# Performance work log

Measured on AMD Instinct MI355X. Metric: run time of the kernel, lower is better.

Reference implementation:

```python
import jax, jax.numpy as jnp
import numpy as np

KERNEL_SIZE = 9
DOMAIN = 8
VTH1 = 1.0
VTH2 = 1.0
VTH3 = 100000.0
BETA1 = min(0.999, 0.9)
BETA2 = min(0.999, 0.9)
BETA3 = min(0.999, 0.95)


def _make_kernels() -> np.ndarray:
    # 16 oriented Gaussian kernels, sigma1=1, sigma2=4, phi = k*2*pi/32, k=0..15
    ks = []
    a = np.linspace(-DOMAIN, DOMAIN, KERNEL_SIZE)
    xs, ys = np.meshgrid(a, a, indexing='xy')  # centered at (0,0)
    coo = np.stack([xs, ys], axis=2)  # [K,K,2]
    l1, l2 = 1.0 ** 2, 4.0 ** 2
    for count in range(16):
        phi = count * 2.0 * np.pi / 32.0
        c, s = np.cos(phi), np.sin(phi)
        cxx = l1 * c * c + l2 * s * s
        cxy = (l1 - l2) * c * s
        cyy = l1 * s * s + l2 * c * c
        cov = np.array([[cxx, cxy], [cxy, cyy]])
        ci = np.linalg.inv(cov)
        cd = np.linalg.det(cov)
        frac = 1.0 / (2.0 * np.pi * np.sqrt(cd))
        # quadratic form: (-coo) @ ci . coo  (matches torch einsum chain)
        q = np.einsum('xyj,jk,xyk->xy', -coo, ci, coo)
        ks.append(frac * np.exp(q / 2.0))
    return np.stack(ks).astype(np.float32)[:, None]  # [16,1,9,9]


def heaviside(v):
    return (v > 0).astype(v.dtype)


def setup_inputs() -> dict:
    key = jax.random.key(0)
    k1, k2, k3 = jax.random.split(key, 3)
    B, T, H, W = 16, 50, 64, 64
    x = jax.random.uniform(k1, (B, T, 1, H, W), dtype=jnp.float32)
    kernels = jnp.asarray(_make_kernels())  # [16,1,9,9], fixed buffer
    fan1 = 16 * H * W
    w1 = jax.random.uniform(k2, (200, fan1), jnp.float32, -1.0, 1.0) / np.sqrt(fan1)
    w2 = jax.random.uniform(k3, (1, 200), jnp.float32, -1.0, 1.0) / np.sqrt(200.0)
    return {"x": x, "kernels": kernels, "w1": w1, "w2": w2}


def reference(x, kernels, w1, w2):
    B, T, C, H, W = x.shape
    pad = KERNEL_SIZE // 2

    def step(carry, xt):
        m1, m2, m3 = carry
        # conv2d, stride 1, same padding -> [B,16,H,W]
        g1 = jax.lax.conv_general_dilated(
            xt, kernels, window_strides=(1, 1),
            padding=[(pad, pad), (pad, pad)],
            dimension_numbers=('NCHW', 'OIHW', 'NCHW'))
        # snntorch Leaky, reset_mechanism='zero': reset from previous mem,
        # then mem = (beta*mem + input) * (1 - reset); spk = H(mem - vth)
        r1 = heaviside(m1 - VTH1)
        m1 = (BETA1 * m1 + g1) * (1.0 - r1)
        z1 = heaviside(m1 - VTH1)
        g2 = z1.reshape(B, -1) @ w1.T  # [B,200]
        r2 = heaviside(m2 - VTH2)
        m2 = (BETA2 * m2 + g2) * (1.0 - r2)
        z2 = heaviside(m2 - VTH2)
        g3 = z2 @ w2.T  # [B,1]
        r3 = heaviside(m3 - VTH3)  # threshold 1e5: never fires
        m3 = (BETA3 * m3 + g3) * (1.0 - r3)
        return (m1, m2, m3), m3

    m1 = jnp.zeros((B, 16, H, W), x.dtype)
    m2 = jnp.zeros((B, 200), x.dtype)
    m3 = jnp.zeros((B, 1), x.dtype)
    xt = jnp.moveaxis(x, 1, 0)  # [T,B,1,H,W]
    _, ys = jax.lax.scan(step, (m1, m2, m3), xt)
    return jnp.moveaxis(ys, 0, 1)  # [B,T,1]
```

## Files before the change

### kernel.cpp

```cpp
#include <hip/hip_runtime.h>
#include <hip/hip_bf16.h>


typedef __attribute__((ext_vector_type(8))) short short8;
typedef __attribute__((ext_vector_type(4))) float f32x4;
typedef __attribute__((ext_vector_type(4))) int   i32x4;

#define B_   16
#define T_   50
#define HW_  4096
#define K1N  65536
#define M_   800
#define N2_  200
#define NP_  256
#define KSPL 64
#define BM2  64
#define BK2  64
#define KCH  (K1N / KSPL)
#define MT2  13
#define SW   84
#define NCONV 512
#define NPERM (200 * 32)

static __device__ __forceinline__ short8 mk8(uint a, uint b, uint c, uint d){
  union { uint u[4]; short8 v; } x;
  x.u[0] = a; x.u[1] = b; x.u[2] = c; x.u[3] = d;
  return x.v;
}
static __device__ __forceinline__ uint fnl(uint a, uint b){ return (a >> 16) | (b << 16); }

template<bool WODD>
static __device__ __forceinline__ void rd5(const uint* p, int dw, uint e[5]){
  if (WODD){
    e[0] = p[dw];
    uint2 a = *(const uint2*)(p + dw + 1);
    uint2 b = *(const uint2*)(p + dw + 3);
    e[1] = a.x; e[2] = a.y; e[3] = b.x; e[4] = b.y;
  } else {
    uint2 a = *(const uint2*)(p + dw);
    uint2 b = *(const uint2*)(p + dw + 2);
    e[0] = a.x; e[1] = a.y; e[2] = b.x; e[3] = b.y;
    e[4] = p[dw + 4];
  }
}

template<bool WODD>
static __device__ __forceinline__ void conv_phase(const uint* T0, const uint* T1,
                                                  int bdw,
                                                  const short8 (&afh)[5],
                                                  const short8 (&afl)[5],
                                                  f32x4& acc0, f32x4& acc1){
  #pragma unroll
  for (int ks = 0; ks < 5; ++ks){
    const int dw = bdw + (SW / 2) * 2 * ks;
    uint h[5], m[5];
    rd5<WODD>(T0, dw, h);
    rd5<WODD>(T1, dw, m);
    short8 bh0 = mk8(h[0], h[1], h[2], h[3]);
    short8 bm0 = mk8(m[0], m[1], m[2], m[3]);
    acc0 = __builtin_amdgcn_mfma_f32_16x16x32_bf16(afh[ks], bh0, acc0, 0, 0, 0);
    acc0 = __builtin_amdgcn_mfma_f32_16x16x32_bf16(afh[ks], bm0, acc0, 0, 0, 0);
    acc0 = __builtin_amdgcn_mfma_f32_16x16x32_bf16(afl[ks], bh0, acc0, 0, 0, 0);
    short8 bh1 = mk8(fnl(h[0], h[1]), fnl(h[1], h[2]), fnl(h[2], h[3]), fnl(h[3], h[4]));
    short8 bm1 = mk8(fnl(m[0], m[1]), fnl(m[1], m[2]), fnl(m[2], m[3]), fnl(m[3], m[4]));
    acc1 = __builtin_amdgcn_mfma_f32_16x16x32_bf16(afh[ks], bh1, acc1, 0, 0, 0);
    acc1 = __builtin_amdgcn_mfma_f32_16x16x32_bf16(afh[ks], bm1, acc1, 0, 0, 0);
    acc1 = __builtin_amdgcn_mfma_f32_16x16x32_bf16(afl[ks], bh1, acc1, 0, 0, 0);
  }
}

__global__ __launch_bounds__(256) void k01_fused(const float* __restrict__ x,
                                                 const float* __restrict__ kern,
                                                 const float* __restrict__ w1,
                                                 unsigned char* __restrict__ zout,
                                                 char* __restrict__ wa,
                                                 char* __restrict__ wb){
  __shared__ __align__(16) ushort smem[9152];
  const int bid = blockIdx.x;
  const int tid = threadIdx.x;

  if (bid >= NCONV){
    char* la = (char*)smem;
    char* lb = la + 2048;
    const int bid2 = bid - NCONV;
    const int n = bid2 >> 5;
    const int strip = bid2 & 31;
    #pragma unroll
    for (int i = 0; i < 8; ++i){
      int lin = tid + 256 * i;
      int ch = lin >> 7, p128 = lin & 127;
      float v = w1[(size_t)n * K1N + ch * 4096 + strip * 128 + p128];
      int s = p128 >> 3, o = p128 & 7, q = ch >> 2, r = ch & 3;
      int kp = o * 256 + s * 16 + q * 4 + r;
      float af = rintf(v * 16384.f);
      float rr = v - af * 0x1p-14f;
      float bf = rintf(rr * 0x1p22f);
      int A = (int)af, Bq = (int)bf;
      if (Bq == 128){ A += 1; Bq = -128; }
      la[kp] = (char)A;
      lb[kp] = (char)Bq;
    }
    __syncthreads();
    const size_t ob = (size_t)n * K1N + strip * 2048;
    *(uint2*)(wa + ob + tid * 8) = *(const uint2*)(la + tid * 8);
    *(uint2*)(wb + ob + tid * 8) = *(const uint2*)(lb + tid * 8);
    return;
  }

  ushort* Ah  = smem;
  ushort* Alo = smem + 2560;
  ushort* Tt  = smem + 5120;

  const int strip = bid & 31;
  const int b = bid >> 5;
  const int w = tid >> 6;
  const int l = tid & 63;
  const int q = l >> 4;
  const int s = l & 15;

  for (int slot = tid; slot < 16 * 160; slot += 256){
    int ch = slot / 160, kk = slot - ch * 160;
    int dy = kk >> 4, dx = kk & 15;
    float v = 0.f;
    if (dy < 9 && dx < 9) v = kern[ch * 81 + dy * 9 + dx];
    __hip_bfloat16 h = __float2bfloat16(v);
    float hf = __bfloat162float(h);
    __hip_bfloat16 lo = __float2bfloat16(v - hf);
    Ah[slot]  = *reinterpret_cast<ushort*>(&h);
    Alo[slot] = *reinterpret_cast<ushort*>(&lo);
  }

  const bool sact = tid < 240;
  const int sr = tid / 20, sc4 = tid - sr * 20;
  const int r0 = 2 * strip - 4;
  const int imr = r0 + sr;
  const bool sin = sact && imr >= 0 && imr < 64 && sc4 >= 1 && sc4 <= 16;
  const float* xb = x + (size_t)b * (T_ * HW_);
  const float* xsrc = xb + (sin ? (imr * 64 + (sc4 - 1) * 4) : 0);

  {
    float4 f0 = make_float4(0.f, 0.f, 0.f, 0.f);
    if (sin) f0 = *(const float4*)(xsrc);
    if (sact){
      float vv[4] = {f0.x, f0.y, f0.z, f0.w};
      ushort sh[4], sm[4];
      #pragma unroll
      for (int ii = 0; ii < 4; ++ii){
        __hip_bfloat16 h = __float2bfloat16(vv[ii]);
        float t1 = vv[ii] - __bfloat162float(h);
        __hip_bfloat16 m = __float2bfloat16(t1);
        sh[ii] = *reinterpret_cast<ushort*>(&h);
        sm[ii] = *reinterpret_cast<ushort*>(&m);
      }
      int eb = sr * SW + sc4 * 4;
      *(ushort4*)(&Tt[0 * 1008 + eb]) = make_ushort4(sh[0], sh[1], sh[2], sh[3]);
      *(ushort4*)(&Tt[1 * 1008 + eb]) = make_ushort4(sm[0], sm[1], sm[2], sm[3]);
    }
  }
  __syncthreads();

  short8 afh[5], afl[5];
  #pragma unroll
  for (int ks = 0; ks < 5; ++ks){
    afh[ks] = *(const short8*)(Ah + s * 160 + ks * 32 + q * 8);
    afl[ks] = *(const short8*)(Alo + s * 160 + ks * 32 + q * 8);
  }

  const int p0 = (s >> 3) + (q >> 1);
  const int bdw = 42 * p0 + 4 * (s & 7) + 4 * (q & 1) + w;
  const bool wodd = (w & 1) != 0;

  float m1v[2][4];
  #pragma unroll
  for (int oi = 0; oi < 2; ++oi)
    #pragma unroll
    for (int r = 0; r < 4; ++r) m1v[oi][r] = 0.f;

  for (int t = 0; t < T_; ++t){
    __syncthreads();
    float4 nfx = make_float4(0.f, 0.f, 0.f, 0.f);
    if (t + 1 < T_ && sin) nfx = *(const float4*)(xsrc + (size_t)(t + 1) * HW_);

    const int bb = t & 1;
    const uint* T0 = (const uint*)&Tt[(bb * 2 + 0) * 1008];
    const uint* T1 = (const uint*)&Tt[(bb * 2 + 1) * 1008];
    f32x4 acc0 = (f32x4)(0.f), acc1 = (f32x4)(0.f);
    if (wodd) conv_phase<true >(T0, T1, bdw, afh, afl, acc0, acc1);
    else      conv_phase<false>(T0, T1, bdw, afh, afl, acc0, acc1);

    const size_t zr = ((size_t)(t * B_ + b)) * K1N + strip * 2048 + s * 16 + q * 4;
    {
      uint zw = 0;
      #pragma unroll
      for (int r = 0; r < 4; ++r){
        float m = m1v[0][r];
        float nm = (m > 1.0f) ? 0.0f : __fadd_rn(__fmul_rn(0.9f, m), acc0[r]);
        m1v[0][r] = nm;
        if (nm > 1.0f) zw |= (1u << (8 * r));
      }
      *(uint*)(zout + zr + (size_t)(2 * w) * 256) = zw;
    }
    {
      uint zw = 0;
      #pragma unroll
      for (int r = 0; r < 4; ++r){
        float m = m1v[1][r];
        float nm = (m > 1.0f) ? 0.0f : __fadd_rn(__fmul_rn(0.9f, m), acc1[r]);
        m1v[1][r] = nm;
        if (nm > 1.0f) zw |= (1u << (8 * r));
      }
      *(uint*)(zout + zr + (size_t)(2 * w + 1) * 256) = zw;
    }

    if (t + 1 < T_ && sact){
      float vv[4] = {nfx.x, nfx.y, nfx.z, nfx.w};
      ushort sh[4], sm[4];
      #pragma unroll
      for (int ii = 0; ii < 4; ++ii){
        __hip_bfloat16 h = __float2bfloat16(vv[ii]);
        float t1 = vv[ii] - __bfloat162float(h);
        __hip_bfloat16 m = __float2bfloat16(t1);
        sh[ii] = *reinterpret_cast<ushort*>(&h);
        sm[ii] = *reinterpret_cast<ushort*>(&m);
      }
      int eb = sr * SW + sc4 * 4;
      *(ushort4*)(&Tt[((bb ^ 1) * 2 + 0) * 1008 + eb]) = make_ushort4(sh[0], sh[1], sh[2], sh[3]);
      *(ushort4*)(&Tt[((bb ^ 1) * 2 + 1) * 1008 + eb]) = make_ushort4(sm[0], sm[1], sm[2], sm[3]);
    }
  }
}

static __device__ __forceinline__ void k2_load(const unsigned char* __restrict__ z,
                                               const char* __restrict__ wa,
                                               const char* __restrict__ wb,
                                               int m0, int kg, int tid,
                                               uint4& pa, uint4 pb[8]){
  {
    int row = tid >> 2, c16 = tid & 3;
    int m = m0 + row;
    pa = make_uint4(0, 0, 0, 0);
    if (m < M_) pa = *(const uint4*)(z + (size_t)m * K1N + kg + c16 * 16);
  }
  #pragma unroll
  for (int i = 0; i < 8; ++i){
    int idx = tid + 256 * i;
    int sel = idx >> 10;
    int r   = (idx >> 2) & 255;
    int c16 = idx & 3;
    const char* src = sel ? wb : wa;
    pb[i] = make_uint4(0, 0, 0, 0);
    if (r < N2_) pb[i] = *(const uint4*)(src + (size_t)r * K1N + kg + c16 * 16);
  }
}

__global__ __launch_bounds__(256, 2) void k2_gemm(const unsigned char* __restrict__ z,
                                                  const char* __restrict__ wa,
                                                  const char* __restrict__ wb,
                                                  float* __restrict__ P){
  __shared__ __align__(16) unsigned char Al[64 * 80];
  __shared__ __align__(16) unsigned char Bw[512 * 80];

  const int bid = blockIdx.x;
  const int L = (bid & 7) * 104 + (bid >> 3);
  const int ks = L / MT2;
  const int mt = L % MT2;
  const int m0 = mt * BM2;
  const int k0 = ks * KCH;
  const int tid = threadIdx.x;
  const int w  = tid >> 6;
  const int l  = tid & 63;
  const int lr = l & 15;
  const int lq = l >> 4;

  const i32x4 zero4 = {0, 0, 0, 0};
  i32x4 accA[4][4], accB[4][4];
  #pragma unroll
  for (int mf = 0; mf < 4; ++mf)
    #pragma unroll
    for (int nf = 0; nf < 4; ++nf){ accA[mf][nf] = zero4; accB[mf][nf] = zero4; }

  uint4 pa, pb[8];
  k2_load(z, wa, wb, m0, k0, tid, pa, pb);

  #pragma unroll 1
  for (int kc = 0; kc < KCH; kc += BK2){
    {
      int row = tid >> 2, c16 = tid & 3;
      *(uint4*)(Al + row * 80 + c16 * 16) = pa;
    }
    #pragma unroll
    for (int i = 0; i < 8; ++i){
      int idx = tid + 256 * i;
      int sel = idx >> 10;
      int r   = (idx >> 2) & 255;
      int c16 = idx & 3;
      *(uint4*)(Bw + (sel * 256 + r) * 80 + c16 * 16) = pb[i];
    }
    __syncthreads();

    if (kc + BK2 < KCH) k2_load(z, wa, wb, m0, k0 + kc + BK2, tid, pa, pb);

    i32x4 af[4], ba[4], bbf[4];
    #pragma unroll
    for (int mf = 0; mf < 4; ++mf)
      af[mf] = *(const i32x4*)(Al + (mf * 16 + lr) * 80 + lq * 16);
    #pragma unroll
    for (int nf = 0; nf < 4; ++nf){
      ba[nf]  = *(const i32x4*)(Bw + (w * 64 + nf * 16 + lr) * 80 + lq * 16);
      bbf[nf] = *(const i32x4*)(Bw + (256 + w * 64 + nf * 16 + lr) * 80 + lq * 16);
    }
    #pragma unroll
    for (int mf = 0; mf < 4; ++mf)
      #pragma unroll
      for (int nf = 0; nf < 4; ++nf){
        accA[mf][nf] = __builtin_amdgcn_mfma_i32_16x16x64_i8(af[mf], ba[nf],  accA[mf][nf], 0, 0, 0);
        accB[mf][nf] = __builtin_amdgcn_mfma_i32_16x16x64_i8(af[mf], bbf[nf], accB[mf][nf], 0, 0, 0);
      }
    __syncthreads();
  }

  #pragma unroll
  for (int mf = 0; mf < 4; ++mf)
    #pragma unroll
    for (int nf = 0; nf < 4; ++nf)
      #pragma unroll
      for (int r = 0; r < 4; ++r){
        int m = m0 + mf * 16 + lq * 4 + r;
        int n = w * 64 + nf * 16 + lr;
        if (m < M_ && n < N2_)
          P[((size_t)ks * M_ + m) * N2_ + n] =
            fmaf((float)accA[mf][nf][r], 0x1p-14f, (float)accB[mf][nf][r] * 0x1p-22f);
      }
}

__global__ __launch_bounds__(256) void k2b_reduce(const float* __restrict__ P,
                                                  float* __restrict__ G2){
  int j = blockIdx.x * 256 + threadIdx.x;
  if (j >= M_ * N2_) return;
  float s = 0.f;
  #pragma unroll
  for (int ks = 0; ks < KSPL; ++ks) s += P[(size_t)ks * (M_ * N2_) + j];
  G2[j] = s;
}

__global__ __launch_bounds__(256) void k3_scan(const float* __restrict__ G2,
                                               const float* __restrict__ w2,
                                               float* __restrict__ out){
  const int b = blockIdx.x;
  const int tid = threadIdx.x;
  const float w = (tid < N2_) ? w2[tid] : 0.f;
  float m2 = 0.f, m3 = 0.f;
  __shared__ float part[4];

  float nxt = (tid < N2_) ? G2[(size_t)b * N2_ + tid] : 0.f;
  for (int t = 0; t < T_; ++t){
    float g2v = nxt;
    if (t < T_ - 1 && tid < N2_) nxt = G2[(size_t)((t + 1) * B_ + b) * N2_ + tid];
    float nm = (m2 > 1.0f) ? 0.f : __fadd_rn(__fmul_rn(0.9f, m2), g2v);
    m2 = nm;
    float s = (m2 > 1.0f) ? w : 0.f;
    #pragma unroll
    for (int off = 32; off > 0; off >>= 1) s += __shfl_down(s, off, 64);
    if ((tid & 63) == 0) part[tid >> 6] = s;
    __syncthreads();
    if (tid == 0){
      float g3 = (part[0] + part[1]) + (part[2] + part[3]);
      m3 = __fadd_rn(__fmul_rn(0.95f, m3), g3);
      out[b * T_ + t] = m3;
    }
    __syncthreads();
  }
}

extern "C" void kernel_launch(void* const* d_in, const int* in_sizes, int n_in,
                              void* d_out, int out_size, void* d_ws, size_t ws_size,
                              hipStream_t stream){
  const float* x    = (const float*)d_in[0];
  const float* kern = (const float*)d_in[1];
  const float* w1   = (const float*)d_in[2];
  const float* w2   = (const float*)d_in[3];
  float* out = (float*)d_out;

  char* p = (char*)d_ws;
  unsigned char* z8 = (unsigned char*)p;     p += (size_t)M_ * K1N;
  char* wa = p;                              p += (size_t)NP_ * K1N;
  char* wb = p;                              p += (size_t)NP_ * K1N;
  float* P  = (float*)p;                     p += (size_t)KSPL * M_ * N2_ * 4;
  float* G2 = (float*)p;                     p += (size_t)M_ * N2_ * 4;

  size_t need = (size_t)(p - (char*)d_ws);
  if (ws_size < need) return;

  hipLaunchKernelGGL(k01_fused,  dim3(NCONV + NPERM), dim3(256), 0, stream,
                     x, kern, w1, z8, wa, wb);
  hipLaunchKernelGGL(k2_gemm,    dim3(MT2 * KSPL), dim3(256), 0, stream, z8, wa, wb, P);
  hipLaunchKernelGGL(k2b_reduce, dim3((M_ * N2_ + 255) / 256), dim3(256), 0, stream, P, G2);
  hipLaunchKernelGGL(k3_scan,    dim3(B_), dim3(256), 0, stream, G2, w2, out);
}
```

Baseline: 156.2 us.

## Split conv timesteps across two wave groups with 512-thread blocks

The fused conv kernel now runs 512 threads per block. Two wave groups each compute the convolution for alternating timesteps using a 4-deep tile ring. The odd-step group passes its accumulators through shared scratch so the even-step group can run the serial membrane update for both steps, which halves the number of loop iterations and barriers on the sequential path. The weight-permute blocks are also rewritten to pack four bytes per thread, and the low-limb kernel fragments are now read from LDS each step instead of kept in registers. The costs are a second barrier per iteration, extra LDS traffic, and only half of the threads doing the scan epilogue.

```diff
diff --git a/kernel.cpp b/kernel.cpp
--- a/kernel.cpp
+++ b/kernel.cpp
@@ -19,8 +19,15 @@
 #define KCH  (K1N / KSPL)
 #define MT2  13
 #define SW   84
+#define TILE 1008
 #define NCONV 512
 #define NPERM (200 * 32)
+
+#define OFF_AH   0
+#define OFF_ALO  5120
+#define OFF_TT   10240
+#define OFF_SCR  26368
+#define SMEM_SZ  34560
 
 static __device__ __forceinline__ short8 mk8(uint a, uint b, uint c, uint d){
   union { uint u[4]; short8 v; } x;
@@ -46,13 +53,13 @@
 
 template<bool WODD>
 static __device__ __forceinline__ void conv_phase(const uint* T0, const uint* T1,
-                                                  int bdw,
+                                                  const ushort* alB, int bdw,
                                                   const short8 (&afh)[5],
-                                                  const short8 (&afl)[5],
                                                   f32x4& acc0, f32x4& acc1){
   #pragma unroll
   for (int ks = 0; ks < 5; ++ks){
-    const int dw = bdw + (SW / 2) * 2 * ks;
+    const int dw = bdw + SW * ks;
+    short8 afl = *(const short8*)(alB + ks * 32);
     uint h[5], m[5];
     rd5<WODD>(T0, dw, h);
     rd5<WODD>(T1, dw, m);
@@ -60,65 +67,96 @@
     short8 bm0 = mk8(m[0], m[1], m[2], m[3]);
     acc0 = __builtin_amdgcn_mfma_f32_16x16x32_bf16(afh[ks], bh0, acc0, 0, 0, 0);
     acc0 = __builtin_amdgcn_mfma_f32_16x16x32_bf16(afh[ks], bm0, acc0, 0, 0, 0);
-    acc0 = __builtin_amdgcn_mfma_f32_16x16x32_bf16(afl[ks], bh0, acc0, 0, 0, 0);
+    acc0 = __builtin_amdgcn_mfma_f32_16x16x32_bf16(afl,     bh0, acc0, 0, 0, 0);
     short8 bh1 = mk8(fnl(h[0], h[1]), fnl(h[1], h[2]), fnl(h[2], h[3]), fnl(h[3], h[4]));
     short8 bm1 = mk8(fnl(m[0], m[1]), fnl(m[1], m[2]), fnl(m[2], m[3]), fnl(m[3], m[4]));
     acc1 = __builtin_amdgcn_mfma_f32_16x16x32_bf16(afh[ks], bh1, acc1, 0, 0, 0);
     acc1 = __builtin_amdgcn_mfma_f32_16x16x32_bf16(afh[ks], bm1, acc1, 0, 0, 0);
-    acc1 = __builtin_amdgcn_mfma_f32_16x16x32_bf16(afl[ks], bh1, acc1, 0, 0, 0);
-  }
-}
-
-__global__ __launch_bounds__(256) void k01_fused(const float* __restrict__ x,
+    acc1 = __builtin_amdgcn_mfma_f32_16x16x32_bf16(afl,     bh1, acc1, 0, 0, 0);
+  }
+}
+
+static __device__ __forceinline__ void stage_tile(ushort* Th, ushort* Tm,
+                                                  int eb, float4 f){
+  float vv[4] = {f.x, f.y, f.z, f.w};
+  ushort sh[4], sm[4];
+  #pragma unroll
+  for (int ii = 0; ii < 4; ++ii){
+    __hip_bfloat16 h = __float2bfloat16(vv[ii]);
+    float t1 = vv[ii] - __bfloat162float(h);
+    __hip_bfloat16 m = __float2bfloat16(t1);
+    sh[ii] = *reinterpret_cast<ushort*>(&h);
+    sm[ii] = *reinterpret_cast<ushort*>(&m);
+  }
+  *(ushort4*)(Th + eb) = make_ushort4(sh[0], sh[1], sh[2], sh[3]);
+  *(ushort4*)(Tm + eb) = make_ushort4(sm[0], sm[1], sm[2], sm[3]);
+}
+
+__global__ __launch_bounds__(512) void k01_fused(const float* __restrict__ x,
                                                  const float* __restrict__ kern,
                                                  const float* __restrict__ w1,
                                                  unsigned char* __restrict__ zout,
                                                  char* __restrict__ wa,
                                                  char* __restrict__ wb){
-  __shared__ __align__(16) ushort smem[9152];
+  __shared__ __align__(16) char smem[SMEM_SZ];
   const int bid = blockIdx.x;
   const int tid = threadIdx.x;
 
   if (bid >= NCONV){
-    char* la = (char*)smem;
-    char* lb = la + 2048;
+    uint* la = (uint*)smem;
+    uint* lb = (uint*)(smem + 2112);
     const int bid2 = bid - NCONV;
     const int n = bid2 >> 5;
     const int strip = bid2 & 31;
-    #pragma unroll
-    for (int i = 0; i < 8; ++i){
-      int lin = tid + 256 * i;
-      int ch = lin >> 7, p128 = lin & 127;
-      float v = w1[(size_t)n * K1N + ch * 4096 + strip * 128 + p128];
-      int s = p128 >> 3, o = p128 & 7, q = ch >> 2, r = ch & 3;
-      int kp = o * 256 + s * 16 + q * 4 + r;
-      float af = rintf(v * 16384.f);
-      float rr = v - af * 0x1p-14f;
-      float bf = rintf(rr * 0x1p22f);
-      int A = (int)af, Bq = (int)bf;
-      if (Bq == 128){ A += 1; Bq = -128; }
-      la[kp] = (char)A;
-      lb[kp] = (char)Bq;
-    }
-    __syncthreads();
-    const size_t ob = (size_t)n * K1N + strip * 2048;
-    *(uint2*)(wa + ob + tid * 8) = *(const uint2*)(la + tid * 8);
-    *(uint2*)(wb + ob + tid * 8) = *(const uint2*)(lb + tid * 8);
+    {
+      const int q = tid >> 7, p128 = tid & 127;
+      const float* src = w1 + (size_t)n * K1N + strip * 128 + p128 + q * 4 * 4096;
+      uint ua = 0, ub = 0;
+      #pragma unroll
+      for (int r = 0; r < 3 + 1; ++r){
+        float v = src[r * 4096];
+        float af = rintf(v * 16384.f);
+        float rr = v - af * 0x1p-14f;
+        float bf = rintf(rr * 0x1p22f);
+        int A = (int)af, Bq = (int)bf;
+        if (Bq == 128){ A += 1; Bq = -128; }
+        ua |= ((uint)(A & 255)) << (8 * r);
+        ub |= ((uint)(Bq & 255)) << (8 * r);
+      }
+      const int o = p128 & 7, s = p128 >> 3;
+      const int u = 64 * o + 4 * s + q + o;
+      la[u] = ua;
+      lb[u] = ub;
+    }
+    __syncthreads();
+    {
+      const int j0 = 2 * (tid & 255);
+      const int o2 = j0 >> 6;
+      const uint* s2 = (tid < 256) ? la : lb;
+      uint v0 = s2[j0 + o2], v1 = s2[j0 + 1 + o2];
+      char* dst = (tid < 256) ? wa : wb;
+      *(uint2*)(dst + (size_t)n * K1N + strip * 2048 + j0 * 4) = make_uint2(v0, v1);
+    }
     return;
   }
 
-  ushort* Ah  = smem;
-  ushort* Alo = smem + 2560;
-  ushort* Tt  = smem + 5120;
+  ushort* Ah  = (ushort*)(smem + OFF_AH);
+  ushort* Alo = (ushort*)(smem + OFF_ALO);
+  float*  scr = (float*)(smem + OFF_SCR);
+  auto tile = [&](int buf, int limb) -> ushort* {
+    return (ushort*)(smem + OFF_TT) + (buf * 2 + limb) * TILE;
+  };
 
   const int strip = bid & 31;
   const int b = bid >> 5;
-  const int w = tid >> 6;
+  const int wv = tid >> 6;
+  const int grp = wv >> 2;
+  const int w = wv & 3;
   const int l = tid & 63;
   const int q = l >> 4;
   const int s = l & 15;
 
-  for (int slot = tid; slot < 16 * 160; slot += 256){
+  for (int slot = tid; slot < 16 * 160; slot += 512){
     int ch = slot / 160, kk = slot - ch * 160;
     int dy = kk >> 4, dx = kk & 15;
     float v = 0.f;
@@ -130,45 +168,30 @@
     Alo[slot] = *reinterpret_cast<ushort*>(&lo);
   }
 
-  const bool sact = tid < 240;
-  const int sr = tid / 20, sc4 = tid - sr * 20;
+  const int st = tid & 255;
+  const bool sact = st < 240;
+  const int sr = st / 20, sc4 = st - sr * 20;
   const int r0 = 2 * strip - 4;
   const int imr = r0 + sr;
   const bool sin = sact && imr >= 0 && imr < 64 && sc4 >= 1 && sc4 <= 16;
   const float* xb = x + (size_t)b * (T_ * HW_);
   const float* xsrc = xb + (sin ? (imr * 64 + (sc4 - 1) * 4) : 0);
-
+  const int eb = sr * SW + sc4 * 4;
+
+  if (sact){
+    float4 f0 = make_float4(0.f, 0.f, 0.f, 0.f);
+    if (sin) f0 = *(const float4*)(xsrc + (size_t)grp * HW_);
+    stage_tile(tile(grp, 0), tile(grp, 1), eb, f0);
+  }
+
+  short8 afh[5];
   {
-    float4 f0 = make_float4(0.f, 0.f, 0.f, 0.f);
-    if (sin) f0 = *(const float4*)(xsrc);
-    if (sact){
-      float vv[4] = {f0.x, f0.y, f0.z, f0.w};
-      ushort sh[4], sm[4];
-      #pragma unroll
-      for (int ii = 0; ii < 4; ++ii){
-        __hip_bfloat16 h = __float2bfloat16(vv[ii]);
-        float t1 = vv[ii] - __bfloat162float(h);
-        __hip_bfloat16 m = __float2bfloat16(t1);
-        sh[ii] = *reinterpret_cast<ushort*>(&h);
-        sm[ii] = *reinterpret_cast<ushort*>(&m);
-      }
-      int eb = sr * SW + sc4 * 4;
-      *(ushort4*)(&Tt[0 * 1008 + eb]) = make_ushort4(sh[0], sh[1], sh[2], sh[3]);
-      *(ushort4*)(&Tt[1 * 1008 + eb]) = make_ushort4(sm[0], sm[1], sm[2], sm[3]);
-    }
-  }
-  __syncthreads();
-
-  short8 afh[5], afl[5];
-  #pragma unroll
-  for (int ks = 0; ks < 5; ++ks){
-    afh[ks] = *(const short8*)(Ah + s * 160 + ks * 32 + q * 8);
-    afl[ks] = *(const short8*)(Alo + s * 160 + ks * 32 + q * 8);
   }
 
   const int p0 = (s >> 3) + (q >> 1);
   const int bdw = 42 * p0 + 4 * (s & 7) + 4 * (q & 1) + w;
   const bool wodd = (w & 1) != 0;
+  const ushort* alB = Alo + s * 160 + q * 8;
 
   float m1v[2][4];
   #pragma unroll
@@ -176,56 +199,91 @@
     #pragma unroll
     for (int r = 0; r < 4; ++r) m1v[oi][r] = 0.f;
 
-  for (int t = 0; t < T_; ++t){
-    __syncthreads();
+  bool afdone = false;
+
+  for (int p = 0; p < T_ / 2; ++p){
+    __syncthreads();
+    if (!afdone){
+      #pragma unroll
+      for (int ks = 0; ks < 5; ++ks)
+        afh[ks] = *(const short8*)(Ah + s * 160 + ks * 32 + q * 8);
+      afdone = true;
+    }
+    const bool pf = (p < T_ / 2 - 1);
     float4 nfx = make_float4(0.f, 0.f, 0.f, 0.f);
-    if (t + 1 < T_ && sin) nfx = *(const float4*)(xsrc + (size_t)(t + 1) * HW_);
-
-    const int bb = t & 1;
-    const uint* T0 = (const uint*)&Tt[(bb * 2 + 0) * 1008];
-    const uint* T1 = (const uint*)&Tt[(bb * 2 + 1) * 1008];
+    if (pf && sin) nfx = *(const float4*)(xsrc + (size_t)(2 * p + 2 + grp) * HW_);
+
+    const int myBuf = (2 * p + grp) & 3;
+    const uint* T0 = (const uint*)tile(myBuf, 0);
+    const uint* T1 = (const uint*)tile(myBuf, 1);
     f32x4 acc0 = (f32x4)(0.f), acc1 = (f32x4)(0.f);
-    if (wodd) conv_phase<true >(T0, T1, bdw, afh, afl, acc0, acc1);
-    else      conv_phase<false>(T0, T1, bdw, afh, afl, acc0, acc1);
-
-    const size_t zr = ((size_t)(t * B_ + b)) * K1N + strip * 2048 + s * 16 + q * 4;
-    {
-      uint zw = 0;
+    if (wodd) conv_phase<true >(T0, T1, alB, bdw, afh, acc0, acc1);
+    else      conv_phase<false>(T0, T1, alB, bdw, afh, acc0, acc1);
+
+    if (grp == 1){
       #pragma unroll
       for (int r = 0; r < 4; ++r){
-        float m = m1v[0][r];
-        float nm = (m > 1.0f) ? 0.0f : __fadd_rn(__fmul_rn(0.9f, m), acc0[r]);
-        m1v[0][r] = nm;
-        if (nm > 1.0f) zw |= (1u << (8 * r));
-      }
-      *(uint*)(zout + zr + (size_t)(2 * w) * 256) = zw;
-    }
-    {
-      uint zw = 0;
-      #pragma unroll
-      for (int r = 0; r < 4; ++r){
-        float m = m1v[1][r];
-        float nm = (m > 1.0f) ? 0.0f : __fadd_rn(__fmul_rn(0.9f, m), acc1[r]);
-        m1v[1][r] = nm;
-        if (nm > 1.0f) zw |= (1u << (8 * r));
-      }
-      *(uint*)(zout + zr + (size_t)(2 * w + 1) * 256) = zw;
-    }
-
-    if (t + 1 < T_ && sact){
-      float vv[4] = {nfx.x, nfx.y, nfx.z, nfx.w};
-      ushort sh[4], sm[4];
-      #pragma unroll
-      for (int ii = 0; ii < 4; ++ii){
-        __hip_bfloat16 h = __float2bfloat16(vv[ii]);
-        float t1 = vv[ii] - __bfloat162float(h);
-        __hip_bfloat16 m = __float2bfloat16(t1);
-        sh[ii] = *reinterpret_cast<ushort*>(&h);
-        sm[ii] = *reinterpret_cast<ushort*>(&m);
-      }
-      int eb = sr * SW + sc4 * 4;
-      *(ushort4*)(&Tt[((bb ^ 1) * 2 + 0) * 1008 + eb]) = make_ushort4(sh[0], sh[1], sh[2], sh[3]);
-      *(ushort4*)(&Tt[((bb ^ 1) * 2 + 1) * 1008 + eb]) = make_ushort4(sm[0], sm[1], sm[2], sm[3]);
+        scr[r * 256 + w * 64 + l]       = acc0[r];
+        scr[(4 + r) * 256 + w * 64 + l] = acc1[r];
+      }
+    }
+    __syncthreads();
+
+    if (grp == 0){
+      float g1v[8];
+      #pragma unroll
+      for (int r = 0; r < 8; ++r) g1v[r] = scr[r * 256 + w * 64 + l];
+      const size_t zb  = ((size_t)(2 * p) * B_ + b) * K1N + strip * 2048 + s * 16 + q * 4;
+      const size_t zb1 = zb + (size_t)B_ * K1N;
+      {
+        uint zw = 0;
+        #pragma unroll
+        for (int r = 0; r < 4; ++r){
+          float m = m1v[0][r];
+          float nm = (m > 1.0f) ? 0.0f : __fadd_rn(__fmul_rn(0.9f, m), acc0[r]);
+          m1v[0][r] = nm;
+          if (nm > 1.0f) zw |= (1u << (8 * r));
+        }
+        *(uint*)(zout + zb + (size_t)(2 * w) * 256) = zw;
+      }
+      {
+        uint zw = 0;
+        #pragma unroll
+        for (int r = 0; r < 4; ++r){
+          float m = m1v[1][r];
+          float nm = (m > 1.0f) ? 0.0f : __fadd_rn(__fmul_rn(0.9f, m), acc1[r]);
+          m1v[1][r] = nm;
+          if (nm > 1.0f) zw |= (1u << (8 * r));
+        }
+        *(uint*)(zout + zb + (size_t)(2 * w + 1) * 256) = zw;
+      }
+      {
+        uint zw = 0;
+        #pragma unroll
+        for (int r = 0; r < 4; ++r){
+          float m = m1v[0][r];
+          float nm = (m > 1.0f) ? 0.0f : __fadd_rn(__fmul_rn(0.9f, m), g1v[r]);
+          m1v[0][r] = nm;
+          if (nm > 1.0f) zw |= (1u << (8 * r));
+        }
+        *(uint*)(zout + zb1 + (size_t)(2 * w) * 256) = zw;
+      }
+      {
+        uint zw = 0;
+        #pragma unroll
+        for (int r = 0; r < 4; ++r){
+          float m = m1v[1][r];
+          float nm = (m > 1.0f) ? 0.0f : __fadd_rn(__fmul_rn(0.9f, m), g1v[4 + r]);
+          m1v[1][r] = nm;
+          if (nm > 1.0f) zw |= (1u << (8 * r));
+        }
+        *(uint*)(zout + zb1 + (size_t)(2 * w + 1) * 256) = zw;
+      }
+    }
+
+    if (pf && sact){
+      const int sb = (2 * p + 2 + grp) & 3;
+      stage_tile(tile(sb, 0), tile(sb, 1), eb, nfx);
     }
   }
 }
@@ -391,7 +449,7 @@
   size_t need = (size_t)(p - (char*)d_ws);
   if (ws_size < need) return;
 
-  hipLaunchKernelGGL(k01_fused,  dim3(NCONV + NPERM), dim3(256), 0, stream,
+  hipLaunchKernelGGL(k01_fused,  dim3(NCONV + NPERM), dim3(512), 0, stream,
                      x, kern, w1, z8, wa, wb);
   hipLaunchKernelGGL(k2_gemm,    dim3(MT2 * KSPL), dim3(256), 0, stream, z8, wa, wb, P);
   hipLaunchKernelGGL(k2b_reduce, dim3((M_ * N2_ + 255) / 256), dim3(256), 0, stream, P, G2);
```

Result: slower. 162.5 us (+4.0%).
